# Optimization experiments

Measured on AMD Instinct MI355X. Metric: run time of the kernel, lower is better.

The kernel has to match this reference:

```python
import jax, jax.numpy as jnp
import numpy as np
import math

N_HEAD = 16
N_KV_HEAD = 4
N_EMBED = 2048
HEAD_DIM = N_EMBED // N_HEAD  # 128
ROPE_BASE = 10000.0


def _rope_tables(T, dim, dtype):
    inv_freq = 1.0 / (ROPE_BASE ** (jnp.arange(0, dim, 2, dtype=jnp.float32) / dim))
    t = jnp.arange(T, dtype=jnp.float32)
    freqs = jnp.outer(t, inv_freq)            # (T, dim/2)
    emb = jnp.concatenate([freqs, freqs], -1) # (T, dim)
    return jnp.cos(emb).astype(dtype), jnp.sin(emb).astype(dtype)


def _rotate_half(x):
    half = x.shape[-1] // 2
    return jnp.concatenate([-x[..., half:], x[..., :half]], axis=-1)


def setup_inputs() -> dict:
    key = jax.random.key(0)
    kx, kq, kk, kv, ko = jax.random.split(key, 5)
    B, T, C = 2, 2048, N_EMBED
    s = 0.02
    return {
        "x": jax.random.normal(kx, (B, T, C), jnp.float32),
        "Wq": jax.random.normal(kq, (N_HEAD * HEAD_DIM, C), jnp.float32) * s,
        "Wk": jax.random.normal(kk, (N_KV_HEAD * HEAD_DIM, C), jnp.float32) * s,
        "Wv": jax.random.normal(kv, (N_KV_HEAD * HEAD_DIM, C), jnp.float32) * s,
        "Wo": jax.random.normal(ko, (C, N_HEAD * HEAD_DIM), jnp.float32) * s,
    }


def reference(x, Wq, Wk, Wv, Wo):
    B, T, C = x.shape
    H, KV, D = N_HEAD, N_KV_HEAD, HEAD_DIM
    rep = H // KV

    q = jnp.einsum('btc,oc->bto', x, Wq).reshape(B, T, H, D).transpose(0, 2, 1, 3)   # (B,H,T,D)
    k = jnp.einsum('btc,oc->bto', x, Wk).reshape(B, T, KV, D).transpose(0, 2, 1, 3)  # (B,KV,T,D)
    v = jnp.einsum('btc,oc->bto', x, Wv).reshape(B, T, KV, D).transpose(0, 2, 1, 3)

    cos, sin = _rope_tables(T, D, x.dtype)  # (T,D) broadcast over (B,h,T,D)
    q = q * cos + _rotate_half(q) * sin
    k = k * cos + _rotate_half(k) * sin

    # GQA: head h attends to kv head h // rep (== repeat_interleave in torch).
    qg = q.reshape(B, KV, rep, T, D)
    scale = 1.0 / math.sqrt(D)
    attn = jnp.einsum('bgrtd,bgsd->bgrts', qg, k) * scale  # (B,KV,rep,T,T)
    causal = jnp.tril(jnp.ones((T, T), dtype=bool))
    attn = jnp.where(causal, attn, -jnp.inf)
    attn = jax.nn.softmax(attn, axis=-1)
    out = jnp.einsum('bgrts,bgsd->bgrtd', attn, v)          # (B,KV,rep,T,D)
    out = out.reshape(B, H, T, D).transpose(0, 2, 1, 3).reshape(B, T, H * D)
    return jnp.einsum('bto,co->btc', out, Wo)
```

## Files before the change

kernel.cpp:

```cpp
#include <hip/hip_runtime.h>
#include <stdint.h>

typedef unsigned short u16;
typedef __attribute__((ext_vector_type(8))) short short8;
typedef __attribute__((ext_vector_type(4))) short short4v;
typedef __attribute__((ext_vector_type(4))) float f32x4;

#define NB_  2
#define NT_  2048
#define NC_  2048
#define NH_  16
#define NKV_ 4
#define HD_  128
#define NM_  (NB_*NT_)

__device__ __forceinline__ u16 f2b(float x) {
  uint32_t u = __float_as_uint(x);
  u += 0x7fffu + ((u >> 16) & 1u);
  return (u16)(u >> 16);
}
__device__ __forceinline__ float b2f(u16 x) {
  return __uint_as_float(((uint32_t)x) << 16);
}
__device__ __forceinline__ uint32_t pk2(float a, float b) {
  return (uint32_t)f2b(a) | ((uint32_t)f2b(b) << 16);
}

typedef __attribute__((address_space(1))) uint32_t* gp1_t;
typedef __attribute__((address_space(3))) uint32_t* lp3_t;
__device__ __forceinline__ void async_ld16(const void* g, void* l) {
  __builtin_amdgcn_global_load_lds((gp1_t)(uintptr_t)g, (lp3_t)(uintptr_t)l, 16, 0, 0);
}

__global__ void f2bf_all(const float* __restrict__ x,  const float* __restrict__ wq,
                         const float* __restrict__ wk, const float* __restrict__ wv,
                         const float* __restrict__ wo,
                         u16* xb, u16* wqb, u16* wkb, u16* wvb, u16* wob) {
  int bid = blockIdx.x;
  const float* src; u16* dst; int base;
  if      (bid < 8192)  { src = x;  dst = xb;  base = bid; }
  else if (bid < 12288) { src = wq; dst = wqb; base = bid - 8192; }
  else if (bid < 13312) { src = wk; dst = wkb; base = bid - 12288; }
  else if (bid < 14336) { src = wv; dst = wvb; base = bid - 13312; }
  else                  { src = wo; dst = wob; base = bid - 14336; }
  int i = base * 256 + threadIdx.x;
  const float4 v = ((const float4*)src)[i];
  short4v o;
  o[0] = (short)f2b(v.x); o[1] = (short)f2b(v.y);
  o[2] = (short)f2b(v.z); o[3] = (short)f2b(v.w);
  *(short4v*)(dst + (size_t)i * 4) = o;
}

__global__ void postk(const u16* __restrict__ qraw, const u16* __restrict__ kraw,
                      const u16* __restrict__ vraw,
                      u16* __restrict__ Qr, u16* __restrict__ Kr, u16* __restrict__ Vt) {
  __shared__ u16 tile[64][72];
  int bid = blockIdx.x;
  if (bid < 20480) {
    const u16* raw; u16* out; int nheads; int tid;
    if (bid < 16384) { raw = qraw; out = Qr; nheads = NH_;  tid = bid * 256 + threadIdx.x; }
    else             { raw = kraw; out = Kr; nheads = NKV_; tid = (bid - 16384) * 256 + threadIdx.x; }
    int j = tid & 63;
    int t = (tid >> 6) & (NT_ - 1);
    int bh = tid >> 17;
    int h = bh % nheads, b = bh / nheads;
    const u16* src = raw + ((size_t)(b * NT_ + t) * nheads + h) * HD_;
    float q0 = b2f(src[j]), q1 = b2f(src[j + 64]);
    float inv = expf(-0.14391156831212787f * (float)j);
    float ang = (float)t * inv;
    float c = cosf(ang), s = sinf(ang);
    u16* dst = out + ((size_t)(b * nheads + h) * NT_ + t) * HD_;
    dst[j]      = f2b(q0 * c - q1 * s);
    dst[j + 64] = f2b(q1 * c + q0 * s);
  } else {
    int idx = bid - 20480;
    int tt = idx & 63, dd = idx >> 6;
    int tid = threadIdx.x;
    int r = tid >> 3, c8 = (tid & 7) * 8;
#pragma unroll
    for (int it = 0; it < 2; ++it) {
      int row = r + it * 32;
      short8 v = *(const short8*)(vraw + (size_t)(tt * 64 + row) * (NKV_ * HD_) + dd * 64 + c8);
      *(short8*)(&tile[row][c8]) = v;
    }
    __syncthreads();
    int b = (tt * 64) >> 11, t0 = (tt * 64) & (NT_ - 1);
    int dl = tid >> 3, t8 = (tid & 7) * 8;
#pragma unroll
    for (int it = 0; it < 2; ++it) {
      int d = dl + it * 32;
      int gcol = dd * 64 + d;
      int kv = gcol >> 7, drow = gcol & 127;
      short8 v;
#pragma unroll
      for (int k = 0; k < 8; ++k) v[k] = (short)tile[t8 + k][d];
      *(short8*)(Vt + ((size_t)(b * NKV_ + kv) * HD_ + drow) * NT_ + t0 + t8) = v;
    }
  }
}

template<int FOUT>
__global__ __launch_bounds__(256, 2)
void gemm128(const u16* __restrict__ A,
             const u16* __restrict__ B1, void* __restrict__ C1, int N1,
             const u16* __restrict__ B2, void* __restrict__ C2, int N2,
             const u16* __restrict__ B3, void* __restrict__ C3, int N3,
             int s1, int s2, int K)
{
  __shared__ u16 As[2 * 128 * 32];
  __shared__ u16 Bs[2 * 128 * 32];
  int bx = blockIdx.x;
  const int by = blockIdx.y;
  const u16* Bmat; void* Cmat; int N;
  if      (bx < s1) { Bmat = B1; Cmat = C1; N = N1; }
  else if (bx < s2) { Bmat = B2; Cmat = C2; N = N2; bx -= s1; }
  else              { Bmat = B3; Cmat = C3; N = N3; bx -= s2; }
  const int m0 = by * 128, n0 = bx * 128;
  const int tid = threadIdx.x;
  const int wave = tid >> 6, lane = tid & 63;
  const int quad = lane >> 4, l15 = lane & 15;
  const int wm = wave >> 1, wn = wave & 1;

  const int p_local = lane >> 3;
  const int s7 = lane & 7;
  const int mlo = s7 >> 2;
  const int gg = (s7 & 3) ^ (p_local & 3);
  const int rowc = p_local * 2 + mlo;
  const int kel = gg * 8;

  const u16* Ag[2]; const u16* Bg[2];
  u16* Al[2]; u16* Bl[2];
#pragma unroll
  for (int q = 0; q < 2; ++q) {
    const int c = wave * 2 + q;
    Ag[q] = A    + (size_t)(m0 + c * 16 + rowc) * K + kel;
    Bg[q] = Bmat + (size_t)(n0 + c * 16 + rowc) * K + kel;
    Al[q] = As + c * 512;
    Bl[q] = Bs + c * 512;
  }

  f32x4 acc[4][4] = {};

  int a_addr[4], b_addr[4];
#pragma unroll
  for (int i = 0; i < 4; ++i) {
    int m = wm * 64 + i * 16 + l15;
    a_addr[i] = ((m >> 1) * 8 + (m & 1) * 4 + (quad ^ ((m >> 1) & 3))) * 8;
    int n = wn * 64 + i * 16 + l15;
    b_addr[i] = ((n >> 1) * 8 + (n & 1) * 4 + (quad ^ ((n >> 1) & 3))) * 8;
  }

  const int nk = K >> 5;
#pragma unroll
  for (int q = 0; q < 2; ++q) {
    async_ld16(Ag[q], Al[q]);
    async_ld16(Bg[q], Bl[q]);
  }

  for (int i = 0; i < nk; ++i) {
    __syncthreads();
    if (i + 1 < nk) {
      const int off = ((i + 1) & 1) * 4096;
      const int k0 = (i + 1) << 5;
#pragma unroll
      for (int q = 0; q < 2; ++q) {
        async_ld16(Ag[q] + k0, Al[q] + off);
        async_ld16(Bg[q] + k0, Bl[q] + off);
      }
    }
    const int off = (i & 1) * 4096;
    short8 af[4], bf[4];
#pragma unroll
    for (int j = 0; j < 4; ++j) af[j] = *(const short8*)(As + off + a_addr[j]);
#pragma unroll
    for (int j = 0; j < 4; ++j) bf[j] = *(const short8*)(Bs + off + b_addr[j]);
#pragma unroll
    for (int mb = 0; mb < 4; ++mb)
#pragma unroll
      for (int nb = 0; nb < 4; ++nb)
        acc[mb][nb] = __builtin_amdgcn_mfma_f32_16x16x32_bf16(af[mb], bf[nb], acc[mb][nb], 0, 0, 0);
  }

#pragma unroll
  for (int mb = 0; mb < 4; ++mb)
#pragma unroll
    for (int nb = 0; nb < 4; ++nb) {
      const int gn = n0 + wn * 64 + nb * 16 + l15;
#pragma unroll
      for (int r = 0; r < 4; ++r) {
        const int gm = m0 + wm * 64 + mb * 16 + quad * 4 + r;
        const float v = acc[mb][nb][r];
        if (FOUT) ((float*)Cmat)[(size_t)gm * N + gn] = v;
        else      ((u16*)Cmat)[(size_t)gm * N + gn] = f2b(v);
      }
    }
}

__global__ __launch_bounds__(256, 2)
void attn_kernel(const u16* __restrict__ Q, const u16* __restrict__ Kg,
                 const u16* __restrict__ Vt, u16* __restrict__ O)
{
  __shared__ u16 Ks[2 * 64 * 128];
  __shared__ u16 Vs[2 * 128 * 64];
  const int pid = blockIdx.x;
  const int h  = blockIdx.y;
  const int b  = blockIdx.z;
  const int kv = h >> 2;
  const int tid = threadIdx.x;
  const int wave = tid >> 6, lane = tid & 63;
  const int quad = lane >> 4, l15 = lane & 15;

  const u16* Kbase = Kg + (size_t)(b * NKV_ + kv) * NT_ * HD_;
  const u16* Vbase = Vt + (size_t)(b * NKV_ + kv) * HD_ * NT_;

  const int krow = lane >> 4, kgs = lane & 15;
  const int vrow = lane >> 3, vgs = lane & 7;
  const float scale = 0.08838834764831845f;

  auto stage = [&](int kt, int pbuf) {
    u16* KsB = Ks + pbuf * 8192;
    u16* VsB = Vs + pbuf * 8192;
#pragma unroll
    for (int q = 0; q < 4; ++q) {
      const int c = wave * 4 + q;
      const int rk = c * 4 + krow;
      const int gk = kgs ^ (rk & 7);
      async_ld16(Kbase + (size_t)(kt * 64 + rk) * HD_ + gk * 8, KsB + c * 512);
      const int rv = c * 8 + vrow;
      const int gv = vgs ^ (rv & 7);
      async_ld16(Vbase + (size_t)rv * NT_ + kt * 64 + gv * 8, VsB + c * 512);
    }
  };

  stage(0, 0);
  int g = 0;

  for (int phase = 0; phase < 2; ++phase) {
    const int qt = phase ? (31 - pid) : pid;

    short8 qf[4];
    {
      const u16* qb = Q + ((size_t)(b * NH_ + h) * NT_ + qt * 64 + wave * 16 + l15) * HD_ + quad * 8;
#pragma unroll
      for (int kb = 0; kb < 4; ++kb) qf[kb] = *(const short8*)(qb + kb * 32);
    }

    f32x4 acc_o[8] = {};
    float m_st = -INFINITY, l_st = 0.f;
    const int tg = qt * 64 + wave * 16 + l15;

    for (int kt = 0; kt <= qt; ++kt) {
      __syncthreads();
      const bool have_next = (kt < qt) || (phase == 0);
      if (have_next) stage((kt < qt) ? kt + 1 : 0, (g + 1) & 1);

      const u16* KsB = Ks + (g & 1) * 8192;
      const u16* VsB = Vs + (g & 1) * 8192;

      f32x4 S[4] = {};
#pragma unroll
      for (int nb = 0; nb < 4; ++nb) {
        const int row = nb * 16 + l15;
#pragma unroll
        for (int kb = 0; kb < 4; ++kb) {
          const int gi = kb * 4 + quad;
          short8 kf = *(const short8*)(KsB + row * 128 + (gi ^ (row & 7)) * 8);
          S[nb] = __builtin_amdgcn_mfma_f32_16x16x32_bf16(kf, qf[kb], S[nb], 0, 0, 0);
        }
      }

      if (kt == qt) {
#pragma unroll
        for (int nb = 0; nb < 4; ++nb)
#pragma unroll
          for (int r = 0; r < 4; ++r) {
            const int sg = kt * 64 + nb * 16 + quad * 4 + r;
            S[nb][r] = (sg > tg) ? -INFINITY : S[nb][r] * scale;
          }
      } else {
#pragma unroll
        for (int nb = 0; nb < 4; ++nb)
#pragma unroll
          for (int r = 0; r < 4; ++r) S[nb][r] *= scale;
      }

      float mx = -INFINITY;
#pragma unroll
      for (int nb = 0; nb < 4; ++nb)
#pragma unroll
        for (int r = 0; r < 4; ++r) mx = fmaxf(mx, S[nb][r]);
      mx = fmaxf(mx, __shfl_xor(mx, 16));
      mx = fmaxf(mx, __shfl_xor(mx, 32));
      const float mn = fmaxf(m_st, mx);
      const float alpha_t = __expf(m_st - mn);
      m_st = mn;
      float rs = 0.f;
#pragma unroll
      for (int nb = 0; nb < 4; ++nb)
#pragma unroll
        for (int r = 0; r < 4; ++r) {
          const float p = __expf(S[nb][r] - mn);
          S[nb][r] = p;
          rs += p;
        }
      rs += __shfl_xor(rs, 16);
      rs += __shfl_xor(rs, 32);
      l_st = l_st * alpha_t + rs;

      float alpha_r[4];
#pragma unroll
      for (int r = 0; r < 4; ++r) alpha_r[r] = __shfl(alpha_t, quad * 4 + r);
#pragma unroll
      for (int db = 0; db < 8; ++db)
#pragma unroll
        for (int r = 0; r < 4; ++r) acc_o[db][r] *= alpha_r[r];

      uint32_t d0[4], d1[4];
#pragma unroll
      for (int nb = 0; nb < 4; ++nb) {
        d0[nb] = pk2(S[nb][0], S[nb][1]);
        d1[nb] = pk2(S[nb][2], S[nb][3]);
      }
      const int srcA = ((quad & 1) * 2) * 16 + l15;
      const int srcB = srcA + 16;
      const bool hi = quad >= 2;
      short8 pf[2];
#pragma unroll
      for (int k2 = 0; k2 < 2; ++k2) {
        const int nbL = k2 * 2, nbH = k2 * 2 + 1;
        uint32_t a0 = (uint32_t)__shfl((int)d0[nbL], srcA);
        uint32_t a1 = (uint32_t)__shfl((int)d1[nbL], srcA);
        uint32_t a2 = (uint32_t)__shfl((int)d0[nbL], srcB);
        uint32_t a3 = (uint32_t)__shfl((int)d1[nbL], srcB);
        uint32_t b0 = (uint32_t)__shfl((int)d0[nbH], srcA);
        uint32_t b1 = (uint32_t)__shfl((int)d1[nbH], srcA);
        uint32_t b2 = (uint32_t)__shfl((int)d0[nbH], srcB);
        uint32_t b3 = (uint32_t)__shfl((int)d1[nbH], srcB);
        uint32_t w[4] = { hi ? b0 : a0, hi ? b1 : a1, hi ? b2 : a2, hi ? b3 : a3 };
        pf[k2] = *(short8*)w;
      }

#pragma unroll
      for (int db = 0; db < 8; ++db) {
        const int row = db * 16 + l15;
#pragma unroll
        for (int k2 = 0; k2 < 2; ++k2) {
          const int gi = k2 * 4 + quad;
          short8 vf = *(const short8*)(VsB + row * 64 + (gi ^ (row & 7)) * 8);
          acc_o[db] = __builtin_amdgcn_mfma_f32_16x16x32_bf16(pf[k2], vf, acc_o[db], 0, 0, 0);
        }
      }
      ++g;
    }

    const float linv = 1.f / l_st;
    float inv_r[4];
#pragma unroll
    for (int r = 0; r < 4; ++r) inv_r[r] = __shfl(linv, quad * 4 + r);
    const size_t orow = ((size_t)b * NT_ + qt * 64 + wave * 16) * (NH_ * HD_);
#pragma unroll
    for (int db = 0; db < 8; ++db)
#pragma unroll
      for (int r = 0; r < 4; ++r)
        O[orow + (size_t)(quad * 4 + r) * (NH_ * HD_) + h * HD_ + db * 16 + l15] =
            f2b(acc_o[db][r] * inv_r[r]);
  }
}

extern "C" void kernel_launch(void* const* d_in, const int* in_sizes, int n_in,
                              void* d_out, int out_size, void* d_ws, size_t ws_size,
                              hipStream_t stream) {
  const float* x  = (const float*)d_in[0];
  const float* Wq = (const float*)d_in[1];
  const float* Wk = (const float*)d_in[2];
  const float* Wv = (const float*)d_in[3];
  const float* Wo = (const float*)d_in[4];
  float* out = (float*)d_out;
  char* ws = (char*)d_ws;
  const size_t MB = (size_t)1 << 20;
  u16* xb   = (u16*)(ws + 0);
  u16* wqb  = (u16*)(ws + 16 * MB);
  u16* wkb  = (u16*)(ws + 24 * MB);
  u16* wvb  = (u16*)(ws + 26 * MB);
  u16* wob  = (u16*)(ws + 28 * MB);
  u16* qraw = (u16*)(ws + 36 * MB);
  u16* kraw = (u16*)(ws + 52 * MB);
  u16* vraw = (u16*)(ws + 56 * MB);
  u16* Qr   = (u16*)(ws + 60 * MB);
  u16* Kr   = (u16*)(ws + 76 * MB);
  u16* Vtb  = (u16*)(ws + 80 * MB);
  u16* Ob   = xb;

  f2bf_all<<<18432, 256, 0, stream>>>(x, Wq, Wk, Wv, Wo, xb, wqb, wkb, wvb, wob);

  gemm128<0><<<dim3(24, 32), 256, 0, stream>>>(xb, wqb, qraw, 2048,
                                               wkb, kraw, 512,
                                               wvb, vraw, 512, 16, 20, 2048);

  postk<<<20992, 256, 0, stream>>>(qraw, kraw, vraw, Qr, Kr, Vtb);

  attn_kernel<<<dim3(16, 16, 2), 256, 0, stream>>>(Qr, Kr, Vtb, Ob);

  gemm128<1><<<dim3(16, 32), 256, 0, stream>>>(Ob, wob, out, 2048,
                                               wob, out, 2048,
                                               wob, out, 2048, 16, 32, 2048);
}
```

Baseline: 301.7 us.

## Rewrite attention with 32x32 MFMA, 64-query-per-wave tiles and batch-based load balancing

The attention kernel moves from 4 waves of 16 queries each, using 16x16x32 MFMAs, to 2 waves of 64 queries each, using 32x32x16 MFMAs. This raises K/V reuse per LDS read and cuts the shuffle overhead of the softmax reductions. Load balancing changes from pairing two q-tiles per block to mirroring the q-tile order across batches. The K LDS swizzle is widened to 16 groups. In exchange, per-lane register use becomes much larger, occupancy drops to a single 128-thread block, and the mirrored schedule may balance work less evenly.

Measured after the change: 412.0 us. +36.6%, slower.

```diff
diff --git a/kernel.cpp b/kernel.cpp
--- a/kernel.cpp
+++ b/kernel.cpp
@@ -5,6 +5,7 @@
 typedef __attribute__((ext_vector_type(8))) short short8;
 typedef __attribute__((ext_vector_type(4))) short short4v;
 typedef __attribute__((ext_vector_type(4))) float f32x4;
+typedef __attribute__((ext_vector_type(16))) float f32x16;
 
 #define NB_  2
 #define NT_  2048
@@ -196,174 +197,193 @@
     }
 }
 
-__global__ __launch_bounds__(256, 2)
+__global__ __launch_bounds__(128, 1)
 void attn_kernel(const u16* __restrict__ Q, const u16* __restrict__ Kg,
                  const u16* __restrict__ Vt, u16* __restrict__ O)
 {
-  __shared__ u16 Ks[2 * 64 * 128];
-  __shared__ u16 Vs[2 * 128 * 64];
-  const int pid = blockIdx.x;
+  __shared__ u16 Ks[2 * 8192];
+  __shared__ u16 Vs[2 * 8192];
+  const int bx = blockIdx.x;
   const int h  = blockIdx.y;
   const int b  = blockIdx.z;
+  const int qi = b ? (15 - bx) : bx;
   const int kv = h >> 2;
   const int tid = threadIdx.x;
   const int wave = tid >> 6, lane = tid & 63;
-  const int quad = lane >> 4, l15 = lane & 15;
+  const int c = lane & 31, hh = lane >> 5;
+  const int qbase = qi * 128 + wave * 64;
 
   const u16* Kbase = Kg + (size_t)(b * NKV_ + kv) * NT_ * HD_;
   const u16* Vbase = Vt + (size_t)(b * NKV_ + kv) * HD_ * NT_;
 
-  const int krow = lane >> 4, kgs = lane & 15;
-  const int vrow = lane >> 3, vgs = lane & 7;
-  const float scale = 0.08838834764831845f;
+  short8 qf[2][8];
+#pragma unroll
+  for (int nt = 0; nt < 2; ++nt) {
+    const u16* qb = Q + ((size_t)(b * NH_ + h) * NT_ + qbase + nt * 32 + c) * HD_ + hh * 8;
+#pragma unroll
+    for (int ks = 0; ks < 8; ++ks) qf[nt][ks] = *(const short8*)(qb + ks * 16);
+  }
+
+  int krow[8], kg8[8], vd[8], vg8[8];
+#pragma unroll
+  for (int qq = 0; qq < 8; ++qq) {
+    const int chunk = 8 * wave + qq;
+    krow[qq] = 4 * chunk + (lane >> 4);
+    kg8[qq]  = ((lane & 15) ^ (krow[qq] & 15)) * 8;
+    vd[qq]   = 8 * chunk + (lane >> 3);
+    vg8[qq]  = ((lane & 7) ^ (vd[qq] & 7)) * 8;
+  }
 
   auto stage = [&](int kt, int pbuf) {
     u16* KsB = Ks + pbuf * 8192;
     u16* VsB = Vs + pbuf * 8192;
 #pragma unroll
-    for (int q = 0; q < 4; ++q) {
-      const int c = wave * 4 + q;
-      const int rk = c * 4 + krow;
-      const int gk = kgs ^ (rk & 7);
-      async_ld16(Kbase + (size_t)(kt * 64 + rk) * HD_ + gk * 8, KsB + c * 512);
-      const int rv = c * 8 + vrow;
-      const int gv = vgs ^ (rv & 7);
-      async_ld16(Vbase + (size_t)rv * NT_ + kt * 64 + gv * 8, VsB + c * 512);
-    }
+    for (int qq = 0; qq < 8; ++qq)
+      async_ld16(Kbase + (size_t)(kt * 64 + krow[qq]) * HD_ + kg8[qq], KsB + (8 * wave + qq) * 512);
+#pragma unroll
+    for (int qq = 0; qq < 8; ++qq)
+      async_ld16(Vbase + (size_t)vd[qq] * NT_ + kt * 64 + vg8[qq], VsB + (8 * wave + qq) * 512);
   };
 
+  f32x16 acc[4][2] = {};
+  float m_st[2] = {-INFINITY, -INFINITY};
+  float l_st[2] = {0.f, 0.f};
+  const float scale = 0.08838834764831845f;
+  const int nkt = 2 * qi + 2;
+
   stage(0, 0);
-  int g = 0;
-
-  for (int phase = 0; phase < 2; ++phase) {
-    const int qt = phase ? (31 - pid) : pid;
-
-    short8 qf[4];
-    {
-      const u16* qb = Q + ((size_t)(b * NH_ + h) * NT_ + qt * 64 + wave * 16 + l15) * HD_ + quad * 8;
-#pragma unroll
-      for (int kb = 0; kb < 4; ++kb) qf[kb] = *(const short8*)(qb + kb * 32);
-    }
-
-    f32x4 acc_o[8] = {};
-    float m_st = -INFINITY, l_st = 0.f;
-    const int tg = qt * 64 + wave * 16 + l15;
-
-    for (int kt = 0; kt <= qt; ++kt) {
-      __syncthreads();
-      const bool have_next = (kt < qt) || (phase == 0);
-      if (have_next) stage((kt < qt) ? kt + 1 : 0, (g + 1) & 1);
-
-      const u16* KsB = Ks + (g & 1) * 8192;
-      const u16* VsB = Vs + (g & 1) * 8192;
-
-      f32x4 S[4] = {};
-#pragma unroll
-      for (int nb = 0; nb < 4; ++nb) {
-        const int row = nb * 16 + l15;
-#pragma unroll
-        for (int kb = 0; kb < 4; ++kb) {
-          const int gi = kb * 4 + quad;
-          short8 kf = *(const short8*)(KsB + row * 128 + (gi ^ (row & 7)) * 8);
-          S[nb] = __builtin_amdgcn_mfma_f32_16x16x32_bf16(kf, qf[kb], S[nb], 0, 0, 0);
+
+  for (int kt = 0; kt < nkt; ++kt) {
+    __syncthreads();
+    if (kt + 1 < nkt) stage(kt + 1, (kt + 1) & 1);
+    if (kt * 64 > qbase + 63) continue;
+
+    const u16* KsB = Ks + (kt & 1) * 8192;
+    const u16* VsB = Vs + (kt & 1) * 8192;
+
+    f32x16 S[2][2] = {};
+#pragma unroll
+    for (int mt = 0; mt < 2; ++mt) {
+      const int row = mt * 32 + c;
+#pragma unroll
+      for (int ks = 0; ks < 8; ++ks) {
+        short8 kfr = *(const short8*)(KsB + (row * 16 + ((2 * ks + hh) ^ (row & 15))) * 8);
+#pragma unroll
+        for (int nt = 0; nt < 2; ++nt)
+          S[mt][nt] = __builtin_amdgcn_mfma_f32_32x32x16_bf16(kfr, qf[nt][ks], S[mt][nt], 0, 0, 0);
+      }
+    }
+
+    const bool diag = (kt * 64 + 63 > qbase);
+    if (diag) {
+#pragma unroll
+      for (int mt = 0; mt < 2; ++mt)
+#pragma unroll
+        for (int nt = 0; nt < 2; ++nt) {
+          const int qg = qbase + nt * 32 + c;
+#pragma unroll
+          for (int r = 0; r < 16; ++r) {
+            const int key = kt * 64 + mt * 32 + (r & 3) + 8 * (r >> 2) + 4 * hh;
+            S[mt][nt][r] = (key > qg) ? -INFINITY : S[mt][nt][r] * scale;
+          }
         }
-      }
-
-      if (kt == qt) {
-#pragma unroll
-        for (int nb = 0; nb < 4; ++nb)
-#pragma unroll
-          for (int r = 0; r < 4; ++r) {
-            const int sg = kt * 64 + nb * 16 + quad * 4 + r;
-            S[nb][r] = (sg > tg) ? -INFINITY : S[nb][r] * scale;
-          }
-      } else {
-#pragma unroll
-        for (int nb = 0; nb < 4; ++nb)
-#pragma unroll
-          for (int r = 0; r < 4; ++r) S[nb][r] *= scale;
-      }
-
+    } else {
+#pragma unroll
+      for (int mt = 0; mt < 2; ++mt)
+#pragma unroll
+        for (int nt = 0; nt < 2; ++nt)
+#pragma unroll
+          for (int r = 0; r < 16; ++r) S[mt][nt][r] *= scale;
+    }
+
+    float alpha[2];
+#pragma unroll
+    for (int nt = 0; nt < 2; ++nt) {
       float mx = -INFINITY;
 #pragma unroll
-      for (int nb = 0; nb < 4; ++nb)
-#pragma unroll
-        for (int r = 0; r < 4; ++r) mx = fmaxf(mx, S[nb][r]);
-      mx = fmaxf(mx, __shfl_xor(mx, 16));
+      for (int mt = 0; mt < 2; ++mt)
+#pragma unroll
+        for (int r = 0; r < 16; ++r) mx = fmaxf(mx, S[mt][nt][r]);
       mx = fmaxf(mx, __shfl_xor(mx, 32));
-      const float mn = fmaxf(m_st, mx);
-      const float alpha_t = __expf(m_st - mn);
-      m_st = mn;
+      const float mn = fmaxf(m_st[nt], mx);
+      alpha[nt] = __expf(m_st[nt] - mn);
+      m_st[nt] = mn;
       float rs = 0.f;
 #pragma unroll
-      for (int nb = 0; nb < 4; ++nb)
-#pragma unroll
-        for (int r = 0; r < 4; ++r) {
-          const float p = __expf(S[nb][r] - mn);
-          S[nb][r] = p;
+      for (int mt = 0; mt < 2; ++mt)
+#pragma unroll
+        for (int r = 0; r < 16; ++r) {
+          const float p = __expf(S[mt][nt][r] - mn);
+          S[mt][nt][r] = p;
           rs += p;
         }
-      rs += __shfl_xor(rs, 16);
       rs += __shfl_xor(rs, 32);
-      l_st = l_st * alpha_t + rs;
-
-      float alpha_r[4];
-#pragma unroll
-      for (int r = 0; r < 4; ++r) alpha_r[r] = __shfl(alpha_t, quad * 4 + r);
-#pragma unroll
-      for (int db = 0; db < 8; ++db)
-#pragma unroll
-        for (int r = 0; r < 4; ++r) acc_o[db][r] *= alpha_r[r];
-
-      uint32_t d0[4], d1[4];
-#pragma unroll
-      for (int nb = 0; nb < 4; ++nb) {
-        d0[nb] = pk2(S[nb][0], S[nb][1]);
-        d1[nb] = pk2(S[nb][2], S[nb][3]);
-      }
-      const int srcA = ((quad & 1) * 2) * 16 + l15;
-      const int srcB = srcA + 16;
-      const bool hi = quad >= 2;
-      short8 pf[2];
-#pragma unroll
-      for (int k2 = 0; k2 < 2; ++k2) {
-        const int nbL = k2 * 2, nbH = k2 * 2 + 1;
-        uint32_t a0 = (uint32_t)__shfl((int)d0[nbL], srcA);
-        uint32_t a1 = (uint32_t)__shfl((int)d1[nbL], srcA);
-        uint32_t a2 = (uint32_t)__shfl((int)d0[nbL], srcB);
-        uint32_t a3 = (uint32_t)__shfl((int)d1[nbL], srcB);
-        uint32_t b0 = (uint32_t)__shfl((int)d0[nbH], srcA);
-        uint32_t b1 = (uint32_t)__shfl((int)d1[nbH], srcA);
-        uint32_t b2 = (uint32_t)__shfl((int)d0[nbH], srcB);
-        uint32_t b3 = (uint32_t)__shfl((int)d1[nbH], srcB);
-        uint32_t w[4] = { hi ? b0 : a0, hi ? b1 : a1, hi ? b2 : a2, hi ? b3 : a3 };
-        pf[k2] = *(short8*)w;
-      }
-
-#pragma unroll
-      for (int db = 0; db < 8; ++db) {
-        const int row = db * 16 + l15;
-#pragma unroll
-        for (int k2 = 0; k2 < 2; ++k2) {
-          const int gi = k2 * 4 + quad;
-          short8 vf = *(const short8*)(VsB + row * 64 + (gi ^ (row & 7)) * 8);
-          acc_o[db] = __builtin_amdgcn_mfma_f32_16x16x32_bf16(pf[k2], vf, acc_o[db], 0, 0, 0);
+      l_st[nt] = l_st[nt] * alpha[nt] + rs;
+    }
+#pragma unroll
+    for (int dmt = 0; dmt < 4; ++dmt)
+#pragma unroll
+      for (int nt = 0; nt < 2; ++nt)
+#pragma unroll
+        for (int r = 0; r < 16; ++r) acc[dmt][nt][r] *= alpha[nt];
+
+    uint32_t P32[2][2][8];
+#pragma unroll
+    for (int mt = 0; mt < 2; ++mt)
+#pragma unroll
+      for (int nt = 0; nt < 2; ++nt)
+#pragma unroll
+        for (int gr = 0; gr < 4; ++gr) {
+          P32[mt][nt][gr * 2 + 0] = pk2(S[mt][nt][4 * gr + 0], S[mt][nt][4 * gr + 1]);
+          P32[mt][nt][gr * 2 + 1] = pk2(S[mt][nt][4 * gr + 2], S[mt][nt][4 * gr + 3]);
         }
-      }
-      ++g;
-    }
-
-    const float linv = 1.f / l_st;
-    float inv_r[4];
-#pragma unroll
-    for (int r = 0; r < 4; ++r) inv_r[r] = __shfl(linv, quad * 4 + r);
-    const size_t orow = ((size_t)b * NT_ + qt * 64 + wave * 16) * (NH_ * HD_);
-#pragma unroll
-    for (int db = 0; db < 8; ++db)
-#pragma unroll
-      for (int r = 0; r < 4; ++r)
-        O[orow + (size_t)(quad * 4 + r) * (NH_ * HD_) + h * HD_ + db * 16 + l15] =
-            f2b(acc_o[db][r] * inv_r[r]);
+    short8 pfrag[4][2];
+#pragma unroll
+    for (int ks = 0; ks < 4; ++ks) {
+      const int mt = ks >> 1, ksl = ks & 1;
+#pragma unroll
+      for (int nt = 0; nt < 2; ++nt) {
+        const uint32_t g0a = P32[mt][nt][(2 * ksl + 0) * 2 + 0];
+        const uint32_t g0b = P32[mt][nt][(2 * ksl + 0) * 2 + 1];
+        const uint32_t g1a = P32[mt][nt][(2 * ksl + 1) * 2 + 0];
+        const uint32_t g1b = P32[mt][nt][(2 * ksl + 1) * 2 + 1];
+        const uint32_t own0 = hh ? g1a : g0a, own1 = hh ? g1b : g0b;
+        const uint32_t snd0 = hh ? g0a : g1a, snd1 = hh ? g0b : g1b;
+        const uint32_t rcv0 = (uint32_t)__shfl_xor((int)snd0, 32);
+        const uint32_t rcv1 = (uint32_t)__shfl_xor((int)snd1, 32);
+        uint32_t w[4];
+        w[0] = hh ? rcv0 : own0;  w[1] = hh ? rcv1 : own1;
+        w[2] = hh ? own0 : rcv0;  w[3] = hh ? own1 : rcv1;
+        pfrag[ks][nt] = *(short8*)w;
+      }
+    }
+
+#pragma unroll
+    for (int dmt = 0; dmt < 4; ++dmt) {
+      const int d = dmt * 32 + c;
+#pragma unroll
+      for (int ks = 0; ks < 4; ++ks) {
+        short8 vfr = *(const short8*)(VsB + (d * 8 + ((2 * ks + hh) ^ (d & 7))) * 8);
+#pragma unroll
+        for (int nt = 0; nt < 2; ++nt)
+          acc[dmt][nt] = __builtin_amdgcn_mfma_f32_32x32x16_bf16(vfr, pfrag[ks][nt], acc[dmt][nt], 0, 0, 0);
+      }
+    }
+  }
+
+#pragma unroll
+  for (int nt = 0; nt < 2; ++nt) {
+    const float inv = 1.f / l_st[nt];
+    u16* orow = O + ((size_t)(b * NT_ + qbase + nt * 32 + c)) * (NH_ * HD_) + h * HD_;
+#pragma unroll
+    for (int dmt = 0; dmt < 4; ++dmt)
+#pragma unroll
+      for (int r4 = 0; r4 < 4; ++r4) {
+        short4v w;
+#pragma unroll
+        for (int j = 0; j < 4; ++j) w[j] = (short)f2b(acc[dmt][nt][4 * r4 + j] * inv);
+        *(short4v*)(orow + dmt * 32 + 8 * r4 + 4 * hh) = w;
+      }
   }
 }
 
@@ -399,7 +419,7 @@
 
   postk<<<20992, 256, 0, stream>>>(qraw, kraw, vraw, Qr, Kr, Vtb);
 
-  attn_kernel<<<dim3(16, 16, 2), 256, 0, stream>>>(Qr, Kr, Vtb, Ob);
+  attn_kernel<<<dim3(16, 16, 2), 128, 0, stream>>>(Qr, Kr, Vtb, Ob);
 
   gemm128<1><<<dim3(16, 32), 256, 0, stream>>>(Ob, wob, out, 2048,
                                                wob, out, 2048,
```
